# Optimization experiments

Measured on AMD Instinct MI355X. Metric: run time of the kernel, lower is better.

The kernel has to match this reference:

```python
import jax, jax.numpy as jnp
import numpy as np

N_NODES = 50000
N_EDGES = 800000
D_IN = 64
D_HID = 64
D_OUT = 16


def setup_inputs() -> dict:
    key = jax.random.key(0)
    ks = jax.random.split(key, 20)
    features = jax.random.normal(ks[0], (N_NODES, D_IN), dtype=jnp.float32)
    src = jax.random.randint(ks[1], (N_EDGES,), 0, N_NODES)
    dst = jax.random.randint(ks[2], (N_EDGES,), 0, N_NODES)

    def lin(k, din, dout):
        bound = 1.0 / np.sqrt(din)
        k1, k2 = jax.random.split(k)
        W = jax.random.uniform(k1, (din, dout), jnp.float32, -bound, bound)
        b = jax.random.uniform(k2, (dout,), jnp.float32, -bound, bound)
        return W, b

    W0a, b0a = lin(ks[3], D_IN, D_HID)
    W0b, b0b = lin(ks[4], D_HID, D_HID)
    W1a, b1a = lin(ks[5], D_HID, D_HID)
    W1b, b1b = lin(ks[6], D_HID, D_HID)
    W2a, b2a = lin(ks[7], D_HID, D_HID)
    W2b, b2b = lin(ks[8], D_HID, D_HID)
    Wout, bout = lin(ks[9], D_HID, D_OUT)
    return {
        "features": features, "src": src, "dst": dst,
        "W0a": W0a, "b0a": b0a, "W0b": W0b, "b0b": b0b,
        "W1a": W1a, "b1a": b1a, "W1b": W1b, "b1b": b1b,
        "W2a": W2a, "b2a": b2a, "W2b": W2b, "b2b": b2b,
        "Wout": Wout, "bout": bout,
    }


def reference(features, src, dst,
              W0a, b0a, W0b, b0b,
              W1a, b1a, W1b, b1b,
              W2a, b2a, W2b, b2b,
              Wout, bout):
    N = features.shape[0]

    def gin_layer(h, Wa, ba, Wb, bb):
        # GINConv 'sum': gather source features along edges, scatter-sum to dst
        agg = jax.ops.segment_sum(h[src], dst, num_segments=N)  # [N, D]
        r = h + agg  # (1 + eps) * h + agg with eps = 0 (DGL default)
        # ApplyNodeFunc MLP: Linear -> ReLU -> Linear
        return jax.nn.relu(r @ Wa + ba) @ Wb + bb

    h = gin_layer(features, W0a, b0a, W0b, b0b)
    h = gin_layer(h, W1a, b1a, W1b, b1b)
    h = gin_layer(h, W2a, b2a, W2b, b2b)
    # dgl.mean_nodes over the single graph -> [1, D_HID]
    hg = jnp.mean(h, axis=0, keepdims=True)
    return hg @ Wout + bout  # [1, D_OUT]
```

## Files before the change

### kernel.cpp

```cpp
#include <hip/hip_runtime.h>
#include <hip/hip_bf16.h>


#define NNODES 50000
#define NEDGES 800000
#define DDIM   64
#define DOUT   16

#define CHUNK  4096
#define NB1    196
#define NBUCK  196
#define NBCVT  6251
#define NB64   782

#define KCAP   1408

typedef unsigned int uint;
typedef unsigned short ushort;
typedef __attribute__((ext_vector_type(8))) short bf16x8;
typedef __attribute__((ext_vector_type(4))) float f32x4;
typedef __attribute__((ext_vector_type(2))) float f32x2;

#define LSTR 72

static __device__ __forceinline__ uint f2bf(float f) {
    uint u = __float_as_uint(f);
    return (u + 0x7fffu + ((u >> 16) & 1u)) >> 16;
}
static __device__ __forceinline__ float bf_lo(uint u) { return __uint_as_float(u << 16); }
static __device__ __forceinline__ float bf_hi(uint u) { return __uint_as_float(u & 0xffff0000u); }


__global__ __launch_bounds__(256) void sort_hist_cvt_kernel(const int* __restrict__ src,
                                                            const int* __restrict__ dst,
                                                            uint* __restrict__ key,
                                                            int* __restrict__ gh,
                                                            const float2* __restrict__ fin,
                                                            uint* __restrict__ hb, int n) {
    __shared__ int h[NBUCK];
    int blk = blockIdx.x;
    if (blk >= NB1) {
        int i = (blk - NB1) * 256 + threadIdx.x;
        if (i < (NNODES + 1) * 32) {
            uint r = 0u;
            if (i < NNODES * 32) {
                float2 v = fin[i];
                r = f2bf(v.x) | (f2bf(v.y) << 16);
            }
            hb[i] = r;
        }
        return;
    }
    for (int i = threadIdx.x; i < NBUCK; i += 256) h[i] = 0;
    __syncthreads();
    int base = blk * CHUNK;
    int end = base + CHUNK < n ? base + CHUNK : n;
    for (int i = base + threadIdx.x; i < end; i += 256) {
        int d = dst[i];
        key[i] = ((uint)d << 16) | (uint)src[i];
        atomicAdd(&h[d >> 8], 1);
    }
    __syncthreads();
    for (int i = threadIdx.x; i < NBUCK; i += 256) gh[blk * NBUCK + i] = h[i];
}


__global__ __launch_bounds__(256) void sort_offsets_a_kernel(const int* __restrict__ gh,
                                                             int* __restrict__ offraw,
                                                             int* __restrict__ tot,
                                                             float* __restrict__ part) {
    __shared__ int s[256];
    int b = blockIdx.x;
    int i = threadIdx.x;
    if (b == 0 && i < 64) part[i] = 0.f;
    int v = (i < NB1) ? gh[i * NBUCK + b] : 0;
    s[i] = v;
    __syncthreads();
    for (int off = 1; off < 256; off <<= 1) {
        int add = (i >= off) ? s[i - off] : 0;
        __syncthreads();
        s[i] += add;
        __syncthreads();
    }
    if (i < NB1) offraw[i * NBUCK + b] = s[i] - v;
    if (i == 255) tot[b] = s[255];
}


__global__ __launch_bounds__(256) void sort_scatter1_kernel(const uint* __restrict__ key,
                                                            const int* __restrict__ offraw,
                                                            const int* __restrict__ tot,
                                                            uint* __restrict__ out, int n) {
    __shared__ int s[256];
    __shared__ int cur[NBUCK];
    int blk = blockIdx.x;
    int i = threadIdx.x;
    int v = (i < NBUCK) ? tot[i] : 0;
    s[i] = v;
    __syncthreads();
    for (int off = 1; off < 256; off <<= 1) {
        int add = (i >= off) ? s[i - off] : 0;
        __syncthreads();
        s[i] += add;
        __syncthreads();
    }
    if (i < NBUCK) cur[i] = (s[i] - v) + offraw[blk * NBUCK + i];
    __syncthreads();
    int base = blk * CHUNK;
    int end = base + CHUNK < n ? base + CHUNK : n;
    for (int j = base + threadIdx.x; j < end; j += 256) {
        uint k = key[j];
        int pos = atomicAdd(&cur[k >> 24], 1);
        out[pos] = k;
    }
}


__global__ __launch_bounds__(256) void sort_bucket_kernel(const uint* __restrict__ in,
                                                          const int* __restrict__ tot,
                                                          int* __restrict__ rowptr,
                                                          uint* __restrict__ out) {
    __shared__ int s[256];
    __shared__ int h[256];
    __shared__ int cur[256];
    __shared__ int slohi[2];
    int b = blockIdx.x;
    int t = threadIdx.x;
    int v = (t < NBUCK) ? tot[t] : 0;
    s[t] = v;
    __syncthreads();
    for (int off = 1; off < 256; off <<= 1) {
        int add = (t >= off) ? s[t - off] : 0;
        __syncthreads();
        s[t] += add;
        __syncthreads();
    }
    if (t == b) { slohi[0] = s[t] - v; slohi[1] = s[t]; }
    h[t] = 0;
    __syncthreads();
    int lo = slohi[0], hi = slohi[1];
    for (int i = lo + t; i < hi; i += 256)
        atomicAdd(&h[(in[i] >> 16) & 255], 1);
    __syncthreads();
    if (t == 0) {
        int run = lo;
        for (int i = 0; i < 256; i++) { cur[i] = run; run += h[i]; }
    }
    __syncthreads();
    int node = (b << 8) + t;
    if (node < NNODES) rowptr[node] = cur[t];
    if (b == NBUCK - 1 && t == 0) rowptr[NNODES] = NEDGES;
    __syncthreads();
    for (int i = lo + t; i < hi; i += 256) {
        uint k = in[i];
        int pos = atomicAdd(&cur[(k >> 16) & 255], 1);
        out[pos] = k;
    }
}


#define ACC4(vv) do { f32x2 u_;                                   \
    u_.x = bf_lo((vv).x); u_.y = bf_hi((vv).x); c0 += u_;         \
    u_.x = bf_lo((vv).y); u_.y = bf_hi((vv).y); c1 += u_;         \
    u_.x = bf_lo((vv).z); u_.y = bf_hi((vv).z); c2 += u_;         \
    u_.x = bf_lo((vv).w); u_.y = bf_hi((vv).w); c3 += u_; } while (0)

__global__ __launch_bounds__(256) void gin_layer_kernel(const uint4* __restrict__ h128,
                                                        const int* __restrict__ rowptr,
                                                        const uint* __restrict__ skey,
                                                        const float* __restrict__ Wa,
                                                        const float* __restrict__ ba,
                                                        const float* __restrict__ Wb,
                                                        const float* __restrict__ bb,
                                                        uint4* __restrict__ out128,
                                                        float* __restrict__ part, int n) {
    __shared__ ushort sW1[64 * LSTR];
    __shared__ ushort sW2[64 * LSTR];
    __shared__ ushort sX[64 * LSTR];
    __shared__ float sba[64], sbb[64];
    __shared__ ushort sSrc[KCAP + 8];
    __shared__ int sRP[65];
    __shared__ float pool[256];

    int t = threadIdx.x;
    int node0 = blockIdx.x * 64;

    for (int i = t; i < 4096; i += 256) {
        int k = i >> 6, nn = i & 63;
        sW1[nn * LSTR + k] = (ushort)f2bf(Wa[i]);
        sW2[nn * LSTR + k] = (ushort)f2bf(Wb[i]);
    }
    if (t < 64) { sba[t] = ba[t]; sbb[t] = bb[t]; }
    if (t < 65) {
        int idx = node0 + t;
        sRP[t] = rowptr[idx < n ? idx : n];
    }
    if (blockIdx.x == 0 && t < 8) {
        uint4 z; z.x = 0; z.y = 0; z.z = 0; z.w = 0;
        out128[(size_t)NNODES * 8 + t] = z;
    }
    int eBase = rowptr[node0];
    int vEnd = node0 + 64 < n ? node0 + 64 : n;
    int nE = rowptr[vEnd] - eBase;
    int nS = nE < KCAP ? nE : KCAP;
    for (int i = t; i < nS; i += 256) sSrc[i] = (ushort)skey[eBase + i];
    __syncthreads();

    int lane = t & 63;
    int w = t >> 6;
    int m0 = w * 16;
    int g = lane >> 3;
    uint p = (uint)(lane & 7);

#pragma unroll
    for (int s = 0; s < 2; s++) {
        int row = m0 + 8 * s + g;
        int v = node0 + row;
        if (v < n) {
            f32x2 c0 = {0.f, 0.f}, c1 = {0.f, 0.f}, c2 = {0.f, 0.f}, c3 = {0.f, 0.f};
            uint4 su = h128[(uint)v * 8u + p];
            ACC4(su);
            int e0r = sRP[row], e1r = sRP[row + 1];
            for (int e = e0r; e < e1r; e += 8) {
                int eo = e - eBase;
                uint k0 = sSrc[eo + 0];
                uint k1 = (e + 1 < e1r) ? (uint)sSrc[eo + 1] : 50000u;
                uint k2 = (e + 2 < e1r) ? (uint)sSrc[eo + 2] : 50000u;
                uint k3 = (e + 3 < e1r) ? (uint)sSrc[eo + 3] : 50000u;
                uint k4 = (e + 4 < e1r) ? (uint)sSrc[eo + 4] : 50000u;
                uint k5 = (e + 5 < e1r) ? (uint)sSrc[eo + 5] : 50000u;
                uint k6 = (e + 6 < e1r) ? (uint)sSrc[eo + 6] : 50000u;
                uint k7 = (e + 7 < e1r) ? (uint)sSrc[eo + 7] : 50000u;
                uint4 v0 = h128[k0 * 8u + p];
                uint4 v1 = h128[k1 * 8u + p];
                uint4 v2 = h128[k2 * 8u + p];
                uint4 v3 = h128[k3 * 8u + p];
                uint4 v4 = h128[k4 * 8u + p];
                uint4 v5 = h128[k5 * 8u + p];
                uint4 v6 = h128[k6 * 8u + p];
                uint4 v7 = h128[k7 * 8u + p];
                ACC4(v0); ACC4(v1); ACC4(v2); ACC4(v3);
                ACC4(v4); ACC4(v5); ACC4(v6); ACC4(v7);
            }
            uint4 o;
            o.x = f2bf(c0.x) | (f2bf(c0.y) << 16);
            o.y = f2bf(c1.x) | (f2bf(c1.y) << 16);
            o.z = f2bf(c2.x) | (f2bf(c2.y) << 16);
            o.w = f2bf(c3.x) | (f2bf(c3.y) << 16);
            *(uint4*)&sX[row * LSTR + (int)p * 8] = o;
        }
    }

    int mc = lane & 15;
    int quad = lane >> 4;

    bf16x8 xa0 = *(const bf16x8*)&sX[(m0 + mc) * LSTR + quad * 8];
    bf16x8 xa1 = *(const bf16x8*)&sX[(m0 + mc) * LSTR + 32 + quad * 8];
    ushort hreg[16];
#pragma unroll
    for (int c = 0; c < 4; c++) {
        bf16x8 b0 = *(const bf16x8*)&sW1[(c * 16 + mc) * LSTR + quad * 8];
        bf16x8 b1 = *(const bf16x8*)&sW1[(c * 16 + mc) * LSTR + 32 + quad * 8];
        f32x4 acc = {0.f, 0.f, 0.f, 0.f};
        acc = __builtin_amdgcn_mfma_f32_16x16x32_bf16(xa0, b0, acc, 0, 0, 0);
        acc = __builtin_amdgcn_mfma_f32_16x16x32_bf16(xa1, b1, acc, 0, 0, 0);
        int col = c * 16 + mc;
        float bias = sba[col];
#pragma unroll
        for (int r = 0; r < 4; r++)
            hreg[c * 4 + r] = (ushort)f2bf(fmaxf(acc[r] + bias, 0.f));
    }
#pragma unroll
    for (int c = 0; c < 4; c++) {
        int col = c * 16 + mc;
#pragma unroll
        for (int r = 0; r < 4; r++)
            sX[(m0 + quad * 4 + r) * LSTR + col] = hreg[c * 4 + r];
    }

    bool rok[4];
#pragma unroll
    for (int r = 0; r < 4; r++) rok[r] = (node0 + m0 + quad * 4 + r) < n;
    float csum[4] = {0.f, 0.f, 0.f, 0.f};

    bf16x8 ha0 = *(const bf16x8*)&sX[(m0 + mc) * LSTR + quad * 8];
    bf16x8 ha1 = *(const bf16x8*)&sX[(m0 + mc) * LSTR + 32 + quad * 8];
#pragma unroll
    for (int c = 0; c < 4; c++) {
        bf16x8 b0 = *(const bf16x8*)&sW2[(c * 16 + mc) * LSTR + quad * 8];
        bf16x8 b1 = *(const bf16x8*)&sW2[(c * 16 + mc) * LSTR + 32 + quad * 8];
        f32x4 acc = {0.f, 0.f, 0.f, 0.f};
        acc = __builtin_amdgcn_mfma_f32_16x16x32_bf16(ha0, b0, acc, 0, 0, 0);
        acc = __builtin_amdgcn_mfma_f32_16x16x32_bf16(ha1, b1, acc, 0, 0, 0);
        int col = c * 16 + mc;
        float bias = sbb[col];
#pragma unroll
        for (int r = 0; r < 4; r++) {
            float val = acc[r] + bias;
            hreg[c * 4 + r] = (ushort)f2bf(val);
            csum[c] += rok[r] ? val : 0.f;
        }
    }
#pragma unroll
    for (int c = 0; c < 4; c++) {
        int col = c * 16 + mc;
#pragma unroll
        for (int r = 0; r < 4; r++)
            sX[(m0 + quad * 4 + r) * LSTR + col] = hreg[c * 4 + r];
    }

#pragma unroll
    for (int i = 0; i < 2; i++) {
        int idx = i * 64 + lane;
        int row16 = idx >> 3, q = idx & 7;
        int row = m0 + row16;
        int gr = node0 + row;
        if (gr < n) out128[(size_t)gr * 8 + q] = *(const uint4*)&sX[row * LSTR + q * 8];
    }

    if (part) {
#pragma unroll
        for (int c = 0; c < 4; c++) {
            csum[c] += __shfl_xor(csum[c], 16);
            csum[c] += __shfl_xor(csum[c], 32);
        }
        if (quad == 0) {
#pragma unroll
            for (int c = 0; c < 4; c++) pool[w * 64 + c * 16 + mc] = csum[c];
        }
        __syncthreads();
        if (t < 64) {
            float s4 = pool[t] + pool[64 + t] + pool[128 + t] + pool[192 + t];
            atomicAdd(&part[t], s4);
        }
    }
}


__global__ __launch_bounds__(64) void final_kernel(const float* __restrict__ part,
                                                   const float* __restrict__ Wout,
                                                   const float* __restrict__ bout,
                                                   float* __restrict__ out) {
    __shared__ float cs[64];
    int t = threadIdx.x;
    cs[t] = part[t] * (1.0f / (float)NNODES);
    __syncthreads();
    if (t < DOUT) {
        float o = bout[t];
        for (int d = 0; d < DDIM; d++) o += cs[d] * Wout[d * DOUT + t];
        out[t] = o;
    }
}


extern "C" void kernel_launch(void* const* d_in, const int* in_sizes, int n_in,
                              void* d_out, int out_size, void* d_ws, size_t ws_size,
                              hipStream_t stream) {
    const float* features = (const float*)d_in[0];
    const int*   src      = (const int*)d_in[1];
    const int*   dst      = (const int*)d_in[2];
    const float* W0a = (const float*)d_in[3];  const float* b0a = (const float*)d_in[4];
    const float* W0b = (const float*)d_in[5];  const float* b0b = (const float*)d_in[6];
    const float* W1a = (const float*)d_in[7];  const float* b1a = (const float*)d_in[8];
    const float* W1b = (const float*)d_in[9];  const float* b1b = (const float*)d_in[10];
    const float* W2a = (const float*)d_in[11]; const float* b2a = (const float*)d_in[12];
    const float* W2b = (const float*)d_in[13]; const float* b2b = (const float*)d_in[14];
    const float* Wout = (const float*)d_in[15]; const float* bout = (const float*)d_in[16];
    float* out = (float*)d_out;

    int* gh     = (int*)d_ws;
    int* offraw = gh + 38416;
    int* tot    = offraw + 38416;
    int* rowptr = tot + 256;
    uint* keybuf = (uint*)(rowptr + 50016);
    uint* buf2   = keybuf + 800000;
    uint* hb0    = buf2 + 800000;
    uint* hb1    = hb0 + (NNODES + 1) * 32;
    float* part  = (float*)(hb1 + (NNODES + 1) * 32);

    sort_hist_cvt_kernel<<<NB1 + NBCVT, 256, 0, stream>>>(src, dst, keybuf, gh,
                                                          (const float2*)features, hb0, NEDGES);
    sort_offsets_a_kernel<<<NBUCK, 256, 0, stream>>>(gh, offraw, tot, part);
    sort_scatter1_kernel<<<NB1, 256, 0, stream>>>(keybuf, offraw, tot, buf2, NEDGES);
    sort_bucket_kernel<<<NBUCK, 256, 0, stream>>>(buf2, tot, rowptr, keybuf);

    gin_layer_kernel<<<NB64, 256, 0, stream>>>((const uint4*)hb0, rowptr, keybuf,
                                               W0a, b0a, W0b, b0b, (uint4*)hb1, nullptr, NNODES);
    gin_layer_kernel<<<NB64, 256, 0, stream>>>((const uint4*)hb1, rowptr, keybuf,
                                               W1a, b1a, W1b, b1b, (uint4*)hb0, nullptr, NNODES);
    gin_layer_kernel<<<NB64, 256, 0, stream>>>((const uint4*)hb0, rowptr, keybuf,
                                               W2a, b2a, W2b, b2b, (uint4*)hb1, part, NNODES);

    final_kernel<<<1, 64, 0, stream>>>(part, Wout, bout, out);
}
```

Baseline: 199.2 us.

## Cut kernel launches: fuse offsets scan, pre-transpose weights, fold final GEMV

Drops the separate offsets-scan kernel: the scatter and bucket kernels now each recompute bucket totals and per-block prefixes straight from the histogram. The first kernel also converts all six weight matrices to transposed bf16 once, so each GIN layer loads them with vector copies instead of converting per block. The final mean and output projection run in the last block of layer 3 through a ticket counter, which removes one more launch. The bucket kernel's serial prefix loop becomes a parallel scan, and feature conversion uses a grid-stride loop with fewer blocks. The cost is redundant histogram reads (196 columns per thread) in two kernels and more fence and atomic traffic.

```diff
diff --git a/kernel.cpp b/kernel.cpp
--- a/kernel.cpp
+++ b/kernel.cpp
@@ -10,8 +10,8 @@
 #define CHUNK  4096
 #define NB1    196
 #define NBUCK  196
-#define NBCVT  6251
 #define NB64   782
+#define CVTB   1024
 
 #define KCAP   1408
 
@@ -30,85 +30,103 @@
 static __device__ __forceinline__ float bf_lo(uint u) { return __uint_as_float(u << 16); }
 static __device__ __forceinline__ float bf_hi(uint u) { return __uint_as_float(u & 0xffff0000u); }
 
-
-__global__ __launch_bounds__(256) void sort_hist_cvt_kernel(const int* __restrict__ src,
-                                                            const int* __restrict__ dst,
-                                                            uint* __restrict__ key,
-                                                            int* __restrict__ gh,
-                                                            const float2* __restrict__ fin,
-                                                            uint* __restrict__ hb, int n) {
+#define ACC4(vv) do { f32x2 u_;                                   \
+    u_.x = bf_lo((vv).x); u_.y = bf_hi((vv).x); c0 += u_;         \
+    u_.x = bf_lo((vv).y); u_.y = bf_hi((vv).y); c1 += u_;         \
+    u_.x = bf_lo((vv).z); u_.y = bf_hi((vv).z); c2 += u_;         \
+    u_.x = bf_lo((vv).w); u_.y = bf_hi((vv).w); c3 += u_; } while (0)
+
+
+__global__ __launch_bounds__(256) void s1_kernel(const int* __restrict__ src,
+                                                 const int* __restrict__ dst,
+                                                 uint* __restrict__ key,
+                                                 int* __restrict__ gh,
+                                                 const float2* __restrict__ fin,
+                                                 uint* __restrict__ hb0,
+                                                 uint* __restrict__ hb1,
+                                                 const float* __restrict__ Wa0,
+                                                 const float* __restrict__ Wb0,
+                                                 const float* __restrict__ Wa1,
+                                                 const float* __restrict__ Wb1,
+                                                 const float* __restrict__ Wa2,
+                                                 const float* __restrict__ Wb2,
+                                                 uint* __restrict__ wWT,
+                                                 float* __restrict__ part,
+                                                 int* __restrict__ ticket) {
     __shared__ int h[NBUCK];
     int blk = blockIdx.x;
-    if (blk >= NB1) {
-        int i = (blk - NB1) * 256 + threadIdx.x;
-        if (i < (NNODES + 1) * 32) {
+    int t = threadIdx.x;
+    if (blk < NB1) {
+        for (int i = t; i < NBUCK; i += 256) h[i] = 0;
+        __syncthreads();
+        int base = blk * CHUNK;
+        int end = base + CHUNK < NEDGES ? base + CHUNK : NEDGES;
+        for (int i = base + t; i < end; i += 256) {
+            int d = dst[i];
+            key[i] = ((uint)d << 16) | (uint)src[i];
+            atomicAdd(&h[d >> 8], 1);
+        }
+        __syncthreads();
+        for (int i = t; i < NBUCK; i += 256) gh[blk * NBUCK + i] = h[i];
+        return;
+    }
+    int m = blk - NB1;
+    if (m < CVTB) {
+        for (int i = m * 256 + t; i < (NNODES + 1) * 32; i += CVTB * 256) {
             uint r = 0u;
             if (i < NNODES * 32) {
                 float2 v = fin[i];
                 r = f2bf(v.x) | (f2bf(v.y) << 16);
             }
-            hb[i] = r;
+            hb0[i] = r;
         }
         return;
     }
-    for (int i = threadIdx.x; i < NBUCK; i += 256) h[i] = 0;
-    __syncthreads();
-    int base = blk * CHUNK;
-    int end = base + CHUNK < n ? base + CHUNK : n;
-    for (int i = base + threadIdx.x; i < end; i += 256) {
-        int d = dst[i];
-        key[i] = ((uint)d << 16) | (uint)src[i];
-        atomicAdd(&h[d >> 8], 1);
-    }
-    __syncthreads();
-    for (int i = threadIdx.x; i < NBUCK; i += 256) gh[blk * NBUCK + i] = h[i];
-}
-
-
-__global__ __launch_bounds__(256) void sort_offsets_a_kernel(const int* __restrict__ gh,
-                                                             int* __restrict__ offraw,
-                                                             int* __restrict__ tot,
-                                                             float* __restrict__ part) {
-    __shared__ int s[256];
-    int b = blockIdx.x;
-    int i = threadIdx.x;
-    if (b == 0 && i < 64) part[i] = 0.f;
-    int v = (i < NB1) ? gh[i * NBUCK + b] : 0;
-    s[i] = v;
-    __syncthreads();
-    for (int off = 1; off < 256; off <<= 1) {
-        int add = (i >= off) ? s[i - off] : 0;
-        __syncthreads();
-        s[i] += add;
-        __syncthreads();
-    }
-    if (i < NB1) offraw[i * NBUCK + b] = s[i] - v;
-    if (i == 255) tot[b] = s[255];
+    m -= CVTB;
+    if (m < 6) {
+        const float* Wm = (m == 0) ? Wa0 : (m == 1) ? Wb0 : (m == 2) ? Wa1
+                        : (m == 3) ? Wb1 : (m == 4) ? Wa2 : Wb2;
+        for (int o = t; o < 2048; o += 256) {
+            int nn = o >> 5, kk = o & 31;
+            wWT[m * 2048 + o] = f2bf(Wm[(2 * kk) * 64 + nn]) |
+                                (f2bf(Wm[(2 * kk + 1) * 64 + nn]) << 16);
+        }
+        return;
+    }
+    if (t < 64) part[t] = 0.f;
+    if (t == 64) *ticket = 0;
+    if (t >= 128 && t < 160) hb1[NNODES * 32 + (t - 128)] = 0u;
 }
 
 
 __global__ __launch_bounds__(256) void sort_scatter1_kernel(const uint* __restrict__ key,
-                                                            const int* __restrict__ offraw,
-                                                            const int* __restrict__ tot,
-                                                            uint* __restrict__ out, int n) {
+                                                            const int* __restrict__ gh,
+                                                            uint* __restrict__ out) {
     __shared__ int s[256];
     __shared__ int cur[NBUCK];
     int blk = blockIdx.x;
-    int i = threadIdx.x;
-    int v = (i < NBUCK) ? tot[i] : 0;
-    s[i] = v;
+    int t = threadIdx.x;
+    int own = 0, total = 0;
+    if (t < NBUCK) {
+        for (int c = 0; c < NB1; c++) {
+            int v = gh[c * NBUCK + t];
+            own += (c < blk) ? v : 0;
+            total += v;
+        }
+    }
+    s[t] = (t < NBUCK) ? total : 0;
     __syncthreads();
     for (int off = 1; off < 256; off <<= 1) {
-        int add = (i >= off) ? s[i - off] : 0;
-        __syncthreads();
-        s[i] += add;
-        __syncthreads();
-    }
-    if (i < NBUCK) cur[i] = (s[i] - v) + offraw[blk * NBUCK + i];
+        int add = (t >= off) ? s[t - off] : 0;
+        __syncthreads();
+        s[t] += add;
+        __syncthreads();
+    }
+    if (t < NBUCK) cur[t] = (s[t] - total) + own;
     __syncthreads();
     int base = blk * CHUNK;
-    int end = base + CHUNK < n ? base + CHUNK : n;
-    for (int j = base + threadIdx.x; j < end; j += 256) {
+    int end = base + CHUNK < NEDGES ? base + CHUNK : NEDGES;
+    for (int j = base + t; j < end; j += 256) {
         uint k = key[j];
         int pos = atomicAdd(&cur[k >> 24], 1);
         out[pos] = k;
@@ -117,17 +135,20 @@
 
 
 __global__ __launch_bounds__(256) void sort_bucket_kernel(const uint* __restrict__ in,
-                                                          const int* __restrict__ tot,
+                                                          const int* __restrict__ gh,
                                                           int* __restrict__ rowptr,
                                                           uint* __restrict__ out) {
     __shared__ int s[256];
-    __shared__ int h[256];
+    __shared__ int hh[256];
     __shared__ int cur[256];
-    __shared__ int slohi[2];
-    int b = blockIdx.x;
+    __shared__ int slo[2];
+    int blk = blockIdx.x;
     int t = threadIdx.x;
-    int v = (t < NBUCK) ? tot[t] : 0;
-    s[t] = v;
+    int total = 0;
+    if (t < NBUCK) {
+        for (int c = 0; c < NB1; c++) total += gh[c * NBUCK + t];
+    }
+    s[t] = (t < NBUCK) ? total : 0;
     __syncthreads();
     for (int off = 1; off < 256; off <<= 1) {
         int add = (t >= off) ? s[t - off] : 0;
@@ -135,21 +156,27 @@
         s[t] += add;
         __syncthreads();
     }
-    if (t == b) { slohi[0] = s[t] - v; slohi[1] = s[t]; }
-    h[t] = 0;
-    __syncthreads();
-    int lo = slohi[0], hi = slohi[1];
+    if (t == blk) { slo[0] = s[t] - total; slo[1] = s[t]; }
+    hh[t] = 0;
+    __syncthreads();
+    int lo = slo[0], hi = slo[1];
     for (int i = lo + t; i < hi; i += 256)
-        atomicAdd(&h[(in[i] >> 16) & 255], 1);
-    __syncthreads();
-    if (t == 0) {
-        int run = lo;
-        for (int i = 0; i < 256; i++) { cur[i] = run; run += h[i]; }
-    }
-    __syncthreads();
-    int node = (b << 8) + t;
+        atomicAdd(&hh[(in[i] >> 16) & 255], 1);
+    __syncthreads();
+    int hv = hh[t];
+    s[t] = hv;
+    __syncthreads();
+    for (int off = 1; off < 256; off <<= 1) {
+        int add = (t >= off) ? s[t - off] : 0;
+        __syncthreads();
+        s[t] += add;
+        __syncthreads();
+    }
+    cur[t] = lo + s[t] - hv;
+    __syncthreads();
+    int node = (blk << 8) + t;
     if (node < NNODES) rowptr[node] = cur[t];
-    if (b == NBUCK - 1 && t == 0) rowptr[NNODES] = NEDGES;
+    if (blk == NBUCK - 1 && t == 0) rowptr[NNODES] = NEDGES;
     __syncthreads();
     for (int i = lo + t; i < hi; i += 256) {
         uint k = in[i];
@@ -159,21 +186,19 @@
 }
 
 
-#define ACC4(vv) do { f32x2 u_;                                   \
-    u_.x = bf_lo((vv).x); u_.y = bf_hi((vv).x); c0 += u_;         \
-    u_.x = bf_lo((vv).y); u_.y = bf_hi((vv).y); c1 += u_;         \
-    u_.x = bf_lo((vv).z); u_.y = bf_hi((vv).z); c2 += u_;         \
-    u_.x = bf_lo((vv).w); u_.y = bf_hi((vv).w); c3 += u_; } while (0)
-
 __global__ __launch_bounds__(256) void gin_layer_kernel(const uint4* __restrict__ h128,
                                                         const int* __restrict__ rowptr,
                                                         const uint* __restrict__ skey,
-                                                        const float* __restrict__ Wa,
+                                                        const uint4* __restrict__ wa4,
+                                                        const uint4* __restrict__ wb4,
                                                         const float* __restrict__ ba,
-                                                        const float* __restrict__ Wb,
                                                         const float* __restrict__ bb,
                                                         uint4* __restrict__ out128,
-                                                        float* __restrict__ part, int n) {
+                                                        float* __restrict__ part,
+                                                        int* __restrict__ ticket,
+                                                        const float* __restrict__ Wout,
+                                                        const float* __restrict__ bout,
+                                                        float* __restrict__ out, int n) {
     __shared__ ushort sW1[64 * LSTR];
     __shared__ ushort sW2[64 * LSTR];
     __shared__ ushort sX[64 * LSTR];
@@ -181,14 +206,15 @@
     __shared__ ushort sSrc[KCAP + 8];
     __shared__ int sRP[65];
     __shared__ float pool[256];
+    __shared__ int lastFlag;
 
     int t = threadIdx.x;
     int node0 = blockIdx.x * 64;
 
-    for (int i = t; i < 4096; i += 256) {
-        int k = i >> 6, nn = i & 63;
-        sW1[nn * LSTR + k] = (ushort)f2bf(Wa[i]);
-        sW2[nn * LSTR + k] = (ushort)f2bf(Wb[i]);
+    for (int i = t; i < 512; i += 256) {
+        int nn = i >> 3, k8 = i & 7;
+        *(uint4*)&sW1[nn * LSTR + k8 * 8] = wa4[nn * 8 + k8];
+        *(uint4*)&sW2[nn * LSTR + k8 * 8] = wb4[nn * 8 + k8];
     }
     if (t < 64) { sba[t] = ba[t]; sbb[t] = bb[t]; }
     if (t < 65) {
@@ -333,22 +359,24 @@
             float s4 = pool[t] + pool[64 + t] + pool[128 + t] + pool[192 + t];
             atomicAdd(&part[t], s4);
         }
-    }
-}
-
-
-__global__ __launch_bounds__(64) void final_kernel(const float* __restrict__ part,
-                                                   const float* __restrict__ Wout,
-                                                   const float* __restrict__ bout,
-                                                   float* __restrict__ out) {
-    __shared__ float cs[64];
-    int t = threadIdx.x;
-    cs[t] = part[t] * (1.0f / (float)NNODES);
-    __syncthreads();
-    if (t < DOUT) {
-        float o = bout[t];
-        for (int d = 0; d < DDIM; d++) o += cs[d] * Wout[d * DOUT + t];
-        out[t] = o;
+        __syncthreads();
+        if (t == 0) {
+            __threadfence();
+            int old = atomicAdd(ticket, 1);
+            lastFlag = (old == NB64 - 1) ? 1 : 0;
+        }
+        __syncthreads();
+        if (lastFlag) {
+            if (t < 64)
+                pool[t] = __hip_atomic_load(&part[t], __ATOMIC_RELAXED,
+                                            __HIP_MEMORY_SCOPE_AGENT) * (1.0f / (float)NNODES);
+            __syncthreads();
+            if (t < DOUT) {
+                float o = bout[t];
+                for (int d = 0; d < DDIM; d++) o += pool[d] * Wout[d * DOUT + t];
+                out[t] = o;
+            }
+        }
     }
 }
 
@@ -369,27 +397,35 @@
     float* out = (float*)d_out;
 
     int* gh     = (int*)d_ws;
-    int* offraw = gh + 38416;
-    int* tot    = offraw + 38416;
-    int* rowptr = tot + 256;
+    int* rowptr = gh + 38416;
     uint* keybuf = (uint*)(rowptr + 50016);
     uint* buf2   = keybuf + 800000;
     uint* hb0    = buf2 + 800000;
     uint* hb1    = hb0 + (NNODES + 1) * 32;
     float* part  = (float*)(hb1 + (NNODES + 1) * 32);
-
-    sort_hist_cvt_kernel<<<NB1 + NBCVT, 256, 0, stream>>>(src, dst, keybuf, gh,
-                                                          (const float2*)features, hb0, NEDGES);
-    sort_offsets_a_kernel<<<NBUCK, 256, 0, stream>>>(gh, offraw, tot, part);
-    sort_scatter1_kernel<<<NB1, 256, 0, stream>>>(keybuf, offraw, tot, buf2, NEDGES);
-    sort_bucket_kernel<<<NBUCK, 256, 0, stream>>>(buf2, tot, rowptr, keybuf);
+    int* ticket  = (int*)(part + 64);
+    uint* wWT    = (uint*)(ticket + 4);
+
+    s1_kernel<<<NB1 + CVTB + 7, 256, 0, stream>>>(src, dst, keybuf, gh,
+                                                  (const float2*)features, hb0, hb1,
+                                                  W0a, W0b, W1a, W1b, W2a, W2b,
+                                                  wWT, part, ticket);
+    sort_scatter1_kernel<<<NB1, 256, 0, stream>>>(keybuf, gh, buf2);
+    sort_bucket_kernel<<<NBUCK, 256, 0, stream>>>(buf2, gh, rowptr, keybuf);
 
     gin_layer_kernel<<<NB64, 256, 0, stream>>>((const uint4*)hb0, rowptr, keybuf,
-                                               W0a, b0a, W0b, b0b, (uint4*)hb1, nullptr, NNODES);
+                                               (const uint4*)(wWT + 0 * 2048),
+                                               (const uint4*)(wWT + 1 * 2048),
+                                               b0a, b0b, (uint4*)hb1,
+                                               nullptr, nullptr, nullptr, nullptr, nullptr, NNODES);
     gin_layer_kernel<<<NB64, 256, 0, stream>>>((const uint4*)hb1, rowptr, keybuf,
-                                               W1a, b1a, W1b, b1b, (uint4*)hb0, nullptr, NNODES);
+                                               (const uint4*)(wWT + 2 * 2048),
+                                               (const uint4*)(wWT + 3 * 2048),
+                                               b1a, b1b, (uint4*)hb0,
+                                               nullptr, nullptr, nullptr, nullptr, nullptr, NNODES);
     gin_layer_kernel<<<NB64, 256, 0, stream>>>((const uint4*)hb0, rowptr, keybuf,
-                                               W2a, b2a, W2b, b2b, (uint4*)hb1, part, NNODES);
-
-    final_kernel<<<1, 64, 0, stream>>>(part, Wout, bout, out);
-}
+                                               (const uint4*)(wWT + 4 * 2048),
+                                               (const uint4*)(wWT + 5 * 2048),
+                                               b2a, b2b, (uint4*)hb1,
+                                               part, ticket, Wout, bout, out, NNODES);
+}
```

Result: slower. 229.4 us (+15.2%).
